# Kernel optimization log

Hardware: AMD Instinct MI355X
Metric: run time of the kernel (lower is better)

## Reference

```python
import jax, jax.numpy as jnp
import numpy as np

B, N, C, E, K, L = 8, 20000, 256, 320000, 3, 2
EPS = 1e-5

def setup_inputs() -> dict:
    key = jax.random.key(0)
    ks = jax.random.split(key, 8)
    features = jax.random.normal(ks[0], (B * N, C), dtype=jnp.float32)
    edge_index = jax.random.randint(ks[1], (2, E), 0, N, dtype=jnp.int64)
    # ChebConv params per layer: K linear weights [C,C] (no per-lin bias) + one bias [C]
    W = jax.random.normal(ks[2], (L, K, C, C), dtype=jnp.float32) * 0.05
    b = jax.random.normal(ks[3], (L, C), dtype=jnp.float32) * 0.05
    # node-mode LayerNorm affine params per layer
    ln_w = jnp.ones((L, C), dtype=jnp.float32)
    ln_b = jnp.zeros((L, C), dtype=jnp.float32)
    return {"features": features, "W": W, "b": b, "ln_w": ln_w, "ln_b": ln_b,
            "edge_index": edge_index, "batch_size": B}


def reference(features, W, b, ln_w, ln_b, edge_index, batch_size):
    n = features.shape[0] // batch_size
    c = features.shape[-1]
    src, dst = edge_index[0], edge_index[1]
    # sym-normalized Laplacian, lambda_max=2: L_hat = 2L/lmax - I = -D^-1/2 A D^-1/2
    deg = jax.ops.segment_sum(jnp.ones_like(src, dtype=features.dtype), src, num_segments=n)
    dis = jnp.where(deg > 0, jax.lax.rsqrt(jnp.where(deg > 0, deg, 1.0)), 0.0)
    norm = -dis[src] * dis[dst]  # [E]
    n_layers, k_order = W.shape[0], W.shape[1]

    def prop(x):  # L_hat @ x via gather-scale-scatter
        return jax.ops.segment_sum(norm[:, None] * x[src], dst, num_segments=n)

    def cheb(x, Wl, bl):
        Tx0 = x
        out = Tx0 @ Wl[0]
        Tx1 = prop(Tx0)
        out = out + Tx1 @ Wl[1]
        for k in range(2, k_order):
            Tx2 = 2.0 * prop(Tx1) - Tx0
            out = out + Tx2 @ Wl[k]
            Tx0, Tx1 = Tx1, Tx2
        return out + bl

    def single(feats):  # [n, c] -> [n, c]
        x = feats
        for i in range(n_layers):
            # NOTE: module passes original features to every layer's conv (faithful)
            x = cheb(feats, W[i], b[i])
            mu = jnp.mean(x, axis=-1, keepdims=True)
            var = jnp.var(x, axis=-1, keepdims=True)
            x = (x - mu) * jax.lax.rsqrt(var + EPS) * ln_w[i] + ln_b[i]
            # dropout p=0.0 -> identity
        return x

    fb = features.reshape(batch_size, n, c)
    return jax.vmap(single)(fb)
```

## Files before the change

kernel.cpp:

```cpp
#include <hip/hip_runtime.h>
#include <stdint.h>

#define BB 8
#define NN 20000
#define CC 256
#define EE 320000
#define KK 3
#define MROWS (BB * NN)
#define ROWU (BB * CC)

__device__ __forceinline__ float bf2f(ushort u) {
    union { uint32_t ui; float f; } v; v.ui = ((uint32_t)u) << 16; return v.f;
}
__device__ __forceinline__ ushort f2bf(float f) {
    union { uint32_t ui; float f; } v; v.f = f;
    uint32_t r = (v.ui + 0x7FFFu + ((v.ui >> 16) & 1u)) >> 16;
    return (ushort)r;
}

typedef __bf16 bf16x8 __attribute__((ext_vector_type(8)));
typedef float  f32x4  __attribute__((ext_vector_type(4)));

__device__ __forceinline__ void gload16(const void* gptr, void* lptr) {
    __builtin_amdgcn_global_load_lds(
        (const __attribute__((address_space(1))) void*)gptr,
        (__attribute__((address_space(3))) void*)lptr, 16, 0, 0);
}

__global__ void detect_k(const int* __restrict__ raw, int* __restrict__ flag) {
    int i = blockIdx.x * 256 + threadIdx.x;
    int v = 0;
    int idx = 2 * i + 1;
    if (i < EE) v = raw[idx];
    unsigned long long m = __ballot(v != 0);
    if ((threadIdx.x & 63) == 0 && m) atomicOr(flag, 1);
}

__global__ void convert_k(const int* __restrict__ raw, const int* __restrict__ flag,
                          int* __restrict__ src, int* __restrict__ dst) {
    int e = blockIdx.x * 256 + threadIdx.x;
    if (e >= EE) return;
    if (*flag == 0) {
        src[e] = raw[2 * e];
        dst[e] = raw[2 * EE + 2 * e];
    } else {
        src[e] = raw[e];
        dst[e] = raw[EE + e];
    }
}

__global__ void count_k(const int* __restrict__ src, const int* __restrict__ dst,
                        int* __restrict__ deg_out, int* __restrict__ cnt_in) {
    int e = blockIdx.x * 256 + threadIdx.x;
    if (e >= EE) return;
    atomicAdd(&deg_out[src[e]], 1);
    atomicAdd(&cnt_in[dst[e]], 1);
}

__global__ void __launch_bounds__(1024) scan_k(const int* __restrict__ cnt_in,
                                               const int* __restrict__ deg_out,
                                               int* __restrict__ row_ptr,
                                               float* __restrict__ dis) {
    __shared__ int wpart[16];
    const int t = threadIdx.x;
    const int lane = t & 63, wid = t >> 6;
    const int base = t * 20;
    int local[20];
    int sum = 0;
#pragma unroll
    for (int i = 0; i < 20; i++) {
        int idx = base + i;
        int v = (idx < NN) ? cnt_in[idx] : 0;
        local[i] = sum;
        sum += v;
    }
    int sc = sum;
#pragma unroll
    for (int off = 1; off < 64; off <<= 1) {
        int u = __shfl_up(sc, off, 64);
        if (lane >= off) sc += u;
    }
    if (lane == 63) wpart[wid] = sc;
    __syncthreads();
    if (wid == 0 && lane < 16) {
        int v = wpart[lane];
#pragma unroll
        for (int off = 1; off < 16; off <<= 1) {
            int u = __shfl_up(v, off, 64);
            if (lane >= off) v += u;
        }
        wpart[lane] = v;
    }
    __syncthreads();
    int wbase = (wid > 0) ? wpart[wid - 1] : 0;
    int tbase = wbase + sc - sum;
#pragma unroll
    for (int i = 0; i < 20; i++) {
        int idx = base + i;
        if (idx < NN) row_ptr[idx] = tbase + local[i];
    }
    if (t == 1023) row_ptr[NN] = tbase + sum;
    for (int i = t; i < NN; i += 1024) {
        int d = deg_out[i];
        dis[i] = (d > 0) ? rsqrtf((float)d) : 0.0f;
    }
}

__global__ void fill_k(const int* __restrict__ src, const int* __restrict__ dst,
                       const int* __restrict__ row_ptr, int* __restrict__ fillc,
                       const float* __restrict__ dis,
                       int* __restrict__ col, float* __restrict__ w) {
    int e = blockIdx.x * 256 + threadIdx.x;
    if (e >= EE) return;
    int s = src[e], d = dst[e];
    int pos = row_ptr[d] + atomicAdd(&fillc[d], 1);
    col[pos] = s;
    w[pos] = -dis[s] * dis[d];
}

__global__ void cvt_k(const float* __restrict__ x, ushort* __restrict__ y) {
    size_t idx = ((size_t)blockIdx.x * 256 + threadIdx.x) * 4;
    int row = (int)(idx >> 8);
    int c = (int)(idx & 255);
    int b = row / NN, n = row - b * NN;
    float4 v = *(const float4*)(x + idx);
    ushort4 o = make_ushort4(f2bf(v.x), f2bf(v.y), f2bf(v.z), f2bf(v.w));
    *(ushort4*)(y + ((size_t)(n * BB + b) * CC + c)) = o;
}

__global__ void wprep_k(const float* __restrict__ W, ushort* __restrict__ wt) {
    int idx = blockIdx.x * 256 + threadIdx.x;
    if (idx >= 256 * 768) return;
    int n = idx / 768, k = idx % 768;
    int sel = k >> 8, kk = k & 255;
    const float* W1 = W + KK * CC * CC;
    float v;
    if (sel == 0)      v = W1[kk * CC + n] - W1[2 * CC * CC + kk * CC + n];
    else if (sel == 1) v = W1[CC * CC + kk * CC + n];
    else               v = 2.0f * W1[2 * CC * CC + kk * CC + n];
    wt[idx] = f2bf(v);
}

__global__ void __launch_bounds__(256) prop_k(const ushort* __restrict__ x,
                                              ushort* __restrict__ y,
                                              const int* __restrict__ row_ptr,
                                              const int* __restrict__ col,
                                              const float* __restrict__ w) {
    const int n = blockIdx.x;
    const int t = threadIdx.x;
    const int beg = row_ptr[n], end = row_ptr[n + 1];
    const ushort* xb = x + t * 8;
    float a0 = 0, a1 = 0, a2 = 0, a3 = 0, a4 = 0, a5 = 0, a6 = 0, a7 = 0;
    int j = beg;
    for (; j + 4 <= end; j += 4) {
        int s0 = col[j], s1 = col[j + 1], s2 = col[j + 2], s3 = col[j + 3];
        float w0 = w[j], w1 = w[j + 1], w2 = w[j + 2], w3 = w[j + 3];
        uint4 v0 = *(const uint4*)(xb + (size_t)s0 * ROWU);
        uint4 v1 = *(const uint4*)(xb + (size_t)s1 * ROWU);
        uint4 v2 = *(const uint4*)(xb + (size_t)s2 * ROWU);
        uint4 v3 = *(const uint4*)(xb + (size_t)s3 * ROWU);
        a0 += w0 * bf2f((ushort)v0.x) + w1 * bf2f((ushort)v1.x) + w2 * bf2f((ushort)v2.x) + w3 * bf2f((ushort)v3.x);
        a1 += w0 * bf2f((ushort)(v0.x >> 16)) + w1 * bf2f((ushort)(v1.x >> 16)) + w2 * bf2f((ushort)(v2.x >> 16)) + w3 * bf2f((ushort)(v3.x >> 16));
        a2 += w0 * bf2f((ushort)v0.y) + w1 * bf2f((ushort)v1.y) + w2 * bf2f((ushort)v2.y) + w3 * bf2f((ushort)v3.y);
        a3 += w0 * bf2f((ushort)(v0.y >> 16)) + w1 * bf2f((ushort)(v1.y >> 16)) + w2 * bf2f((ushort)(v2.y >> 16)) + w3 * bf2f((ushort)(v3.y >> 16));
        a4 += w0 * bf2f((ushort)v0.z) + w1 * bf2f((ushort)v1.z) + w2 * bf2f((ushort)v2.z) + w3 * bf2f((ushort)v3.z);
        a5 += w0 * bf2f((ushort)(v0.z >> 16)) + w1 * bf2f((ushort)(v1.z >> 16)) + w2 * bf2f((ushort)(v2.z >> 16)) + w3 * bf2f((ushort)(v3.z >> 16));
        a6 += w0 * bf2f((ushort)v0.w) + w1 * bf2f((ushort)v1.w) + w2 * bf2f((ushort)v2.w) + w3 * bf2f((ushort)v3.w);
        a7 += w0 * bf2f((ushort)(v0.w >> 16)) + w1 * bf2f((ushort)(v1.w >> 16)) + w2 * bf2f((ushort)(v2.w >> 16)) + w3 * bf2f((ushort)(v3.w >> 16));
    }
    for (; j < end; j++) {
        int s = col[j];
        float wt = w[j];
        uint4 v = *(const uint4*)(xb + (size_t)s * ROWU);
        a0 += wt * bf2f((ushort)v.x);
        a1 += wt * bf2f((ushort)(v.x >> 16));
        a2 += wt * bf2f((ushort)v.y);
        a3 += wt * bf2f((ushort)(v.y >> 16));
        a4 += wt * bf2f((ushort)v.z);
        a5 += wt * bf2f((ushort)(v.z >> 16));
        a6 += wt * bf2f((ushort)v.w);
        a7 += wt * bf2f((ushort)(v.w >> 16));
    }
    uint4 o;
    o.x = (uint32_t)f2bf(a0) | ((uint32_t)f2bf(a1) << 16);
    o.y = (uint32_t)f2bf(a2) | ((uint32_t)f2bf(a3) << 16);
    o.z = (uint32_t)f2bf(a4) | ((uint32_t)f2bf(a5) << 16);
    o.w = (uint32_t)f2bf(a6) | ((uint32_t)f2bf(a7) << 16);
    *(uint4*)(y + (size_t)n * ROWU + t * 8) = o;
}

__global__ void __launch_bounds__(256) gemm_k(const ushort* __restrict__ a0,
                                              const ushort* __restrict__ a1,
                                              const ushort* __restrict__ a2,
                                              const ushort* __restrict__ wt,
                                              float* __restrict__ out) {
    __shared__ ushort As[128 * 32];
    __shared__ ushort Bs[128 * 32];
    const int tid = threadIdx.x;
    const int wid = tid >> 6, lane = tid & 63;
    const int wrow = wid >> 1, wcol = wid & 1;
    const int row0 = blockIdx.x * 128, col0 = blockIdx.y * 128;
    const int quad = lane >> 4, l16 = lane & 15;

    f32x4 acc[4][4] = {};

    for (int kt = 0; kt < 24; kt++) {
        const ushort* ab = (kt < 8) ? a0 : ((kt < 16) ? a1 : a2);
        const int kl = (kt & 7) * 32;
        const int kg = kt * 32;
        __syncthreads();
#pragma unroll
        for (int q = 0; q < 2; q++) {
            int c = wid * 128 + q * 64 + lane;
            int m = c >> 2, kq = (c & 3) * 8;
            gload16(ab + (size_t)(row0 + m) * CC + kl + kq,
                    &As[(wid * 128 + q * 64) * 8]);
            gload16(wt + (size_t)(col0 + m) * 768 + kg + kq,
                    &Bs[(wid * 128 + q * 64) * 8]);
        }
        __syncthreads();

        bf16x8 af[4], bfr[4];
#pragma unroll
        for (int mt = 0; mt < 4; mt++)
            af[mt] = *(const bf16x8*)&As[(wrow * 64 + mt * 16 + l16) * 32 + quad * 8];
#pragma unroll
        for (int nt = 0; nt < 4; nt++)
            bfr[nt] = *(const bf16x8*)&Bs[(wcol * 64 + nt * 16 + l16) * 32 + quad * 8];
#pragma unroll
        for (int mt = 0; mt < 4; mt++)
#pragma unroll
            for (int nt = 0; nt < 4; nt++)
                acc[mt][nt] = __builtin_amdgcn_mfma_f32_16x16x32_bf16(
                    af[mt], bfr[nt], acc[mt][nt], 0, 0, 0);
    }

#pragma unroll
    for (int mt = 0; mt < 4; mt++) {
#pragma unroll
        for (int nt = 0; nt < 4; nt++) {
#pragma unroll
            for (int r = 0; r < 4; r++) {
                int m = row0 + wrow * 64 + mt * 16 + quad * 4 + r;
                int n = m >> 3, b = m & 7;
                size_t orow = (size_t)b * NN + n;
                size_t colo = (size_t)col0 + wcol * 64 + nt * 16 + l16;
                out[orow * CC + colo] = acc[mt][nt][r];
            }
        }
    }
}

__global__ void __launch_bounds__(256) ln_k(float* __restrict__ out,
                                            const float* __restrict__ bias,
                                            const float* __restrict__ lnw,
                                            const float* __restrict__ lnb) {
    int wid = threadIdx.x >> 6, lane = threadIdx.x & 63;
    size_t row = (size_t)blockIdx.x * 4 + wid;
    float* p = out + row * CC + lane * 4;
    float4 v = *(float4*)p;
    float4 bb = *(const float4*)(bias + lane * 4);
    v.x += bb.x; v.y += bb.y; v.z += bb.z; v.w += bb.w;
    float s = v.x + v.y + v.z + v.w;
    float sq = v.x * v.x + v.y * v.y + v.z * v.z + v.w * v.w;
    for (int off = 32; off; off >>= 1) {
        s += __shfl_xor(s, off, 64);
        sq += __shfl_xor(sq, off, 64);
    }
    float mean = s * (1.0f / CC);
    float var = sq * (1.0f / CC) - mean * mean;
    float rs = rsqrtf(var + 1e-5f);
    float4 lw = *(const float4*)(lnw + lane * 4);
    float4 lb = *(const float4*)(lnb + lane * 4);
    v.x = (v.x - mean) * rs * lw.x + lb.x;
    v.y = (v.y - mean) * rs * lw.y + lb.y;
    v.z = (v.z - mean) * rs * lw.z + lb.z;
    v.w = (v.w - mean) * rs * lw.w + lb.w;
    *(float4*)p = v;
}

extern "C" void kernel_launch(void* const* d_in, const int* in_sizes, int n_in,
                              void* d_out, int out_size, void* d_ws, size_t ws_size,
                              hipStream_t stream) {
    const float* feats = (const float*)d_in[0];
    const float* W     = (const float*)d_in[1];
    const float* bvec  = (const float*)d_in[2];
    const float* lnw   = (const float*)d_in[3];
    const float* lnb   = (const float*)d_in[4];
    const int*   eidx  = (const int*)d_in[5];
    float* outp = (float*)d_out;

    int* flag    = (int*)d_ws;
    int* deg_out = flag + 64;
    int* cnt_in  = deg_out + NN;
    int* fillc   = cnt_in + NN;
    int* row_ptr = fillc + NN;
    int* srcw    = row_ptr + (NN + 64);
    int* dstw    = srcw + EE;
    int* colw    = dstw + EE;
    float* disw  = (float*)(colw + EE);
    float* ww    = disw + (NN + 64);
    uintptr_t bf_base = ((uintptr_t)(ww + EE) + 255) & ~(uintptr_t)255;
    ushort* featsb = (ushort*)bf_base;
    ushort* tx1b   = featsb + (size_t)MROWS * CC;
    ushort* p2b    = tx1b + (size_t)MROWS * CC;
    ushort* wcat   = p2b + (size_t)MROWS * CC;

    hipMemsetAsync(flag, 0, (size_t)(64 + 3 * NN) * sizeof(int), stream);

    int eb = (EE + 255) / 256;
    detect_k<<<eb, 256, 0, stream>>>(eidx, flag);
    convert_k<<<eb, 256, 0, stream>>>(eidx, flag, srcw, dstw);
    count_k<<<eb, 256, 0, stream>>>(srcw, dstw, deg_out, cnt_in);
    scan_k<<<1, 1024, 0, stream>>>(cnt_in, deg_out, row_ptr, disw);
    fill_k<<<eb, 256, 0, stream>>>(srcw, dstw, row_ptr, fillc, disw, colw, ww);

    cvt_k<<<MROWS * CC / 1024, 256, 0, stream>>>(feats, featsb);
    wprep_k<<<(256 * 768 + 255) / 256, 256, 0, stream>>>(W, wcat);

    prop_k<<<NN, 256, 0, stream>>>(featsb, tx1b, row_ptr, colw, ww);
    prop_k<<<NN, 256, 0, stream>>>(tx1b, p2b, row_ptr, colw, ww);

    gemm_k<<<dim3(MROWS / 128, CC / 128), 256, 0, stream>>>(featsb, tx1b, p2b, wcat, outp);

    ln_k<<<MROWS / 4, 256, 0, stream>>>(outp, bvec + CC, lnw + CC, lnb + CC);
}
```

Before: 972.2 us.

## Fuse bias and LayerNorm into GEMM epilogue with full-width row tiles

```diff
diff --git a/kernel.cpp b/kernel.cpp
--- a/kernel.cpp
+++ b/kernel.cpp
@@ -189,18 +189,22 @@
     *(uint4*)(y + (size_t)n * ROWU + t * 8) = o;
 }
 
-__global__ void __launch_bounds__(256) gemm_k(const ushort* __restrict__ a0,
-                                              const ushort* __restrict__ a1,
-                                              const ushort* __restrict__ a2,
-                                              const ushort* __restrict__ wt,
-                                              float* __restrict__ out) {
-    __shared__ ushort As[128 * 32];
-    __shared__ ushort Bs[128 * 32];
+__global__ void __launch_bounds__(256) gemmln_k(const ushort* __restrict__ a0,
+                                                const ushort* __restrict__ a1,
+                                                const ushort* __restrict__ a2,
+                                                const ushort* __restrict__ wt,
+                                                const float* __restrict__ bias,
+                                                const float* __restrict__ lnw,
+                                                const float* __restrict__ lnb,
+                                                float* __restrict__ out) {
+    __shared__ ushort As[64 * 32];
+    __shared__ ushort Bs[256 * 32];
+    __shared__ float reds[64][4];
+    __shared__ float redq[64][4];
     const int tid = threadIdx.x;
     const int wid = tid >> 6, lane = tid & 63;
-    const int wrow = wid >> 1, wcol = wid & 1;
-    const int row0 = blockIdx.x * 128, col0 = blockIdx.y * 128;
     const int quad = lane >> 4, l16 = lane & 15;
+    const int row0 = blockIdx.x * 64;
 
     f32x4 acc[4][4] = {};
 
@@ -209,24 +213,26 @@
         const int kl = (kt & 7) * 32;
         const int kg = kt * 32;
         __syncthreads();
-#pragma unroll
-        for (int q = 0; q < 2; q++) {
-            int c = wid * 128 + q * 64 + lane;
+        {
+            int c = wid * 64 + lane;
             int m = c >> 2, kq = (c & 3) * 8;
-            gload16(ab + (size_t)(row0 + m) * CC + kl + kq,
-                    &As[(wid * 128 + q * 64) * 8]);
-            gload16(wt + (size_t)(col0 + m) * 768 + kg + kq,
-                    &Bs[(wid * 128 + q * 64) * 8]);
+            gload16(ab + (size_t)(row0 + m) * CC + kl + kq, &As[(wid * 64) * 8]);
+        }
+#pragma unroll
+        for (int q = 0; q < 4; q++) {
+            int c = wid * 256 + q * 64 + lane;
+            int m = c >> 2, kq = (c & 3) * 8;
+            gload16(wt + (size_t)m * 768 + kg + kq, &Bs[(wid * 256 + q * 64) * 8]);
         }
         __syncthreads();
 
         bf16x8 af[4], bfr[4];
 #pragma unroll
         for (int mt = 0; mt < 4; mt++)
-            af[mt] = *(const bf16x8*)&As[(wrow * 64 + mt * 16 + l16) * 32 + quad * 8];
+            af[mt] = *(const bf16x8*)&As[(mt * 16 + l16) * 32 + quad * 8];
 #pragma unroll
         for (int nt = 0; nt < 4; nt++)
-            bfr[nt] = *(const bf16x8*)&Bs[(wcol * 64 + nt * 16 + l16) * 32 + quad * 8];
+            bfr[nt] = *(const bf16x8*)&Bs[(wid * 64 + nt * 16 + l16) * 32 + quad * 8];
 #pragma unroll
         for (int mt = 0; mt < 4; mt++)
 #pragma unroll
@@ -235,48 +241,56 @@
                     af[mt], bfr[nt], acc[mt][nt], 0, 0, 0);
     }
 
+    float bv[4], lwv[4], lbv[4];
+#pragma unroll
+    for (int nt = 0; nt < 4; nt++) {
+        int c = wid * 64 + nt * 16 + l16;
+        bv[nt] = bias[c]; lwv[nt] = lnw[c]; lbv[nt] = lnb[c];
+    }
 #pragma unroll
     for (int mt = 0; mt < 4; mt++) {
 #pragma unroll
-        for (int nt = 0; nt < 4; nt++) {
-#pragma unroll
-            for (int r = 0; r < 4; r++) {
-                int m = row0 + wrow * 64 + mt * 16 + quad * 4 + r;
-                int n = m >> 3, b = m & 7;
-                size_t orow = (size_t)b * NN + n;
-                size_t colo = (size_t)col0 + wcol * 64 + nt * 16 + l16;
-                out[orow * CC + colo] = acc[mt][nt][r];
+        for (int r = 0; r < 4; r++) {
+            float s = 0.0f, q = 0.0f;
+#pragma unroll
+            for (int nt = 0; nt < 4; nt++) {
+                float v = acc[mt][nt][r] + bv[nt];
+                s += v; q += v * v;
             }
-        }
-    }
-}
-
-__global__ void __launch_bounds__(256) ln_k(float* __restrict__ out,
-                                            const float* __restrict__ bias,
-                                            const float* __restrict__ lnw,
-                                            const float* __restrict__ lnb) {
-    int wid = threadIdx.x >> 6, lane = threadIdx.x & 63;
-    size_t row = (size_t)blockIdx.x * 4 + wid;
-    float* p = out + row * CC + lane * 4;
-    float4 v = *(float4*)p;
-    float4 bb = *(const float4*)(bias + lane * 4);
-    v.x += bb.x; v.y += bb.y; v.z += bb.z; v.w += bb.w;
-    float s = v.x + v.y + v.z + v.w;
-    float sq = v.x * v.x + v.y * v.y + v.z * v.z + v.w * v.w;
-    for (int off = 32; off; off >>= 1) {
-        s += __shfl_xor(s, off, 64);
-        sq += __shfl_xor(sq, off, 64);
-    }
-    float mean = s * (1.0f / CC);
-    float var = sq * (1.0f / CC) - mean * mean;
-    float rs = rsqrtf(var + 1e-5f);
-    float4 lw = *(const float4*)(lnw + lane * 4);
-    float4 lb = *(const float4*)(lnb + lane * 4);
-    v.x = (v.x - mean) * rs * lw.x + lb.x;
-    v.y = (v.y - mean) * rs * lw.y + lb.y;
-    v.z = (v.z - mean) * rs * lw.z + lb.z;
-    v.w = (v.w - mean) * rs * lw.w + lb.w;
-    *(float4*)p = v;
+#pragma unroll
+            for (int off = 1; off < 16; off <<= 1) {
+                s += __shfl_xor(s, off, 64);
+                q += __shfl_xor(q, off, 64);
+            }
+            if (l16 == 0) {
+                int m = mt * 16 + quad * 4 + r;
+                reds[m][wid] = s;
+                redq[m][wid] = q;
+            }
+        }
+    }
+    __syncthreads();
+#pragma unroll
+    for (int mt = 0; mt < 4; mt++) {
+#pragma unroll
+        for (int r = 0; r < 4; r++) {
+            int ml = mt * 16 + quad * 4 + r;
+            float s = reds[ml][0] + reds[ml][1] + reds[ml][2] + reds[ml][3];
+            float q = redq[ml][0] + redq[ml][1] + redq[ml][2] + redq[ml][3];
+            float mean = s * (1.0f / CC);
+            float var = q * (1.0f / CC) - mean * mean;
+            float rs = rsqrtf(var + 1e-5f);
+            int m = row0 + ml;
+            int n = m >> 3, b = m & 7;
+            size_t orow = (size_t)b * NN + n;
+#pragma unroll
+            for (int nt = 0; nt < 4; nt++) {
+                int c = wid * 64 + nt * 16 + l16;
+                float v = (acc[mt][nt][r] + bv[nt] - mean) * rs * lwv[nt] + lbv[nt];
+                out[orow * CC + c] = v;
+            }
+        }
+    }
 }
 
 extern "C" void kernel_launch(void* const* d_in, const int* in_sizes, int n_in,
@@ -321,7 +335,6 @@
     prop_k<<<NN, 256, 0, stream>>>(featsb, tx1b, row_ptr, colw, ww);
     prop_k<<<NN, 256, 0, stream>>>(tx1b, p2b, row_ptr, colw, ww);
 
-    gemm_k<<<dim3(MROWS / 128, CC / 128), 256, 0, stream>>>(featsb, tx1b, p2b, wcat, outp);
-
-    ln_k<<<MROWS / 4, 256, 0, stream>>>(outp, bvec + CC, lnw + CC, lnb + CC);
-}
+    gemmln_k<<<MROWS / 64, 256, 0, stream>>>(featsb, tx1b, p2b, wcat,
+                                             bvec + CC, lnw + CC, lnb + CC, outp);
+}
```

Result: faster. 938.3 us (-3.5%).
